# Performance work log

Measured on AMD Instinct MI355X. Metric: run time of the kernel, lower is better.

## Reference

```python
import jax, jax.numpy as jnp
import numpy as np
from math import log, ceil

BUFFER = 1
N_AHEAD = 1


def _num_weights(beta_raw):
    # matches torch: beta_max = beta.max(); min(ceil(log(0.01, beta_max)) + 1, 100)
    beta = np.asarray(jax.nn.sigmoid(beta_raw)) * 0.9999
    beta_max = float(beta.max())
    return int(min(ceil(log(0.01, beta_max)) + 1, 100))


def _garch_sigma(x, alpha_raw, beta_raw, omega_raw, num_weights, buffer, n_ahead):
    alpha = jax.nn.sigmoid(alpha_raw)          # [1, N]
    beta = jax.nn.sigmoid(beta_raw) * 0.9999   # [1, N]
    omega = jax.nn.sigmoid(omega_raw)          # [N]
    T, N = x.shape
    omega2 = omega ** 2
    w0 = omega2 / (1.0 - beta)                 # [1, N] -> GARCH long-run term
    # FIR taps: cumprod(beta)/beta then flip -> [beta^{nw-1}, ..., beta^1, beta^0]
    exps = jnp.arange(num_weights - 1, -1, -1, dtype=x.dtype)[:, None]  # [nw, 1]
    weight = beta ** exps                                               # [nw, N]
    if buffer > 0:
        weight = jnp.concatenate([weight, jnp.zeros((buffer, N), x.dtype)], axis=0)
    K = num_weights + buffer
    x2 = (x * x).T[None]                       # [1, N, T]
    kern = weight.T[:, None, :]                # [N, 1, K]  depthwise kernel
    # torch conv1d = cross-correlation; same for lax.conv_general_dilated
    a = jax.lax.conv_general_dilated(
        x2, kern, window_strides=(1,), padding=[(K - 1, K - 1)],
        dimension_numbers=('NCH', 'OIH', 'NCH'), feature_group_count=N)
    a = a[0, :, :T].T                          # [T, N] causal weighted sum of x^2
    var = w0 + alpha * a                       # [T, N]
    if n_ahead > 1:
        a_b = jax.lax.stop_gradient(jnp.clip(alpha + beta, 0.0, 0.99))
        a_b_n = a_b ** n_ahead
        co2 = (1.0 - a_b_n) / (1.0 - a_b) / n_ahead
        co1 = (1.0 - co2) / (1.0 - a_b)
        var = co1 * omega2 + co2 * var
    return jnp.sqrt(var)


def setup_inputs() -> dict:
    key = jax.random.key(0)
    k1, k2, k3, k4 = jax.random.split(key, 4)
    T, N = 8192, 2048
    x = jax.random.normal(k1, (T, N), jnp.float32) * 0.02      # daily-return scale
    alpha_raw = jax.random.uniform(k2, (1, N), jnp.float32, -4.0, -1.0)
    beta_raw = jax.random.uniform(k3, (1, N), jnp.float32, 0.0, 4.0)
    omega_raw = jax.random.uniform(k4, (N,), jnp.float32, -4.0, -2.0)
    return {"x": x, "alpha_raw": alpha_raw, "beta_raw": beta_raw, "omega_raw": omega_raw}


def reference(x, alpha_raw, beta_raw, omega_raw):
    nw = _num_weights(beta_raw)
    return _garch_sigma(x, alpha_raw, beta_raw, omega_raw, nw, BUFFER, N_AHEAD)
```

## Files before the change

kernel.cpp:

```cpp
#include <hip/hip_runtime.h>
#include <math.h>

#define TPB    256
#define COLS   32
#define SEGLEN 32
#define SEGS   8
#define HSEGS  4
#define QSEGS  (SEGS + HSEGS)
#define TSPAN  (SEGS * SEGLEN)
#define HALO   (HSEGS * SEGLEN)

__global__ __launch_bounds__(TPB, 6) void garch_sigma_kernel(
    const float* __restrict__ x,
    const float* __restrict__ alpha_raw,
    const float* __restrict__ beta_raw,
    const float* __restrict__ omega_raw,
    float*       __restrict__ out,
    int T, int N) {

    __shared__ float Qs[QSEGS][COLS];

    const int tid = threadIdx.x;
    const int col = tid & (COLS - 1);
    const int k   = tid >> 5;
    const int n   = blockIdx.x * COLS + col;
    const int t0  = blockIdx.y * TSPAN;

    const int  nc     = (n < N) ? n : (N - 1);
    const bool col_ok = (n < N);

    const float alpha = 1.f / (1.f + expf(-alpha_raw[nc]));
    const float beta  = (1.f / (1.f + expf(-beta_raw[nc]))) * 0.9999f;
    const float om    = 1.f / (1.f + expf(-omega_raw[nc]));
    const float w0    = om * om / (1.f - beta);

    const size_t rs = (size_t)N;
    const float* __restrict__ xc = x + nc;

    const int g0 = t0 + k * SEGLEN;
    float p[SEGLEN];
    if (t0 + TSPAN <= T) {
        #pragma unroll
        for (int i = 0; i < SEGLEN; ++i)
            p[i] = xc[(size_t)(g0 + i) * rs];
    } else {
        #pragma unroll
        for (int i = 0; i < SEGLEN; ++i)
            p[i] = (g0 + i < T) ? xc[(size_t)(g0 + i) * rs] : 0.f;
    }

    if (k < HSEGS) {
        const int h0 = t0 - HALO + k * SEGLEN;
        float q = 0.f;
        if (h0 >= 0) {
            #pragma unroll
            for (int b = 0; b < 2; ++b) {
                float h[16];
                #pragma unroll
                for (int i = 0; i < 16; ++i)
                    h[i] = xc[(size_t)(h0 + b * 16 + i) * rs];
                #pragma unroll
                for (int i = 0; i < 16; ++i)
                    q = fmaf(beta, q, h[i] * h[i]);
            }
        } else {
            #pragma unroll
            for (int i = 0; i < SEGLEN; ++i) {
                const int gt = h0 + i;
                const float v = (gt >= 0) ? xc[(size_t)gt * rs] : 0.f;
                q = fmaf(beta, q, v * v);
            }
        }
        Qs[k][col] = q;
    }

    {
        float q = 0.f;
        #pragma unroll
        for (int i = 0; i < SEGLEN; ++i) {
            const float s = p[i] * p[i];
            p[i] = s;
            q = fmaf(beta, q, s);
        }
        Qs[HSEGS + k][col] = q;
    }

    __syncthreads();

    float b32;
    {
        const float b2 = beta * beta;
        const float b4 = b2 * b2;
        const float b8 = b4 * b4;
        const float b16 = b8 * b8;
        b32 = b16 * b16;
    }
    float a = 0.f;
    const int nq = k + HSEGS;
    for (int u = 0; u < nq; ++u)
        a = fmaf(b32, a, Qs[u][col]);

    if (col_ok) {
        float* op = out + (size_t)g0 * rs + nc;
        if (t0 + TSPAN <= T) {
            #pragma unroll
            for (int i = 0; i < SEGLEN; ++i) {
                const float sg = sqrtf(fmaf(alpha, a, w0));
                __builtin_nontemporal_store(sg, op + (size_t)i * rs);
                a = fmaf(beta, a, p[i]);
            }
        } else {
            #pragma unroll
            for (int i = 0; i < SEGLEN; ++i) {
                const float sg = sqrtf(fmaf(alpha, a, w0));
                if (g0 + i < T)
                    __builtin_nontemporal_store(sg, op + (size_t)i * rs);
                a = fmaf(beta, a, p[i]);
            }
        }
    }
}

extern "C" void kernel_launch(void* const* d_in, const int* in_sizes, int n_in,
                              void* d_out, int out_size, void* d_ws, size_t ws_size,
                              hipStream_t stream) {
    const float* x   = (const float*)d_in[0];
    const float* ar  = (const float*)d_in[1];
    const float* br  = (const float*)d_in[2];
    const float* orw = (const float*)d_in[3];
    float* out = (float*)d_out;

    const int N = in_sizes[1];
    const int T = in_sizes[0] / N;

    dim3 grid((N + COLS - 1) / COLS, (T + TSPAN - 1) / TSPAN);
    hipLaunchKernelGGL(garch_sigma_kernel, grid, dim3(TPB), 0, stream,
                       x, ar, br, orw, out, T, N);
}
```

Measured before the change: 29.92 us.

## Double segment length and spread halo loading evenly across all warps

Each thread now processes 64 time steps instead of 32, so each block covers 512 steps and the 128-step halo is a smaller share of the loads. The halo is split into 16-step pieces, one per warp, so no warp carries extra halo work and the load stays balanced. The prefix combine uses beta^16 for halo pieces and beta^64 for body segments. In exchange, register use roughly doubles (64-element array), the occupancy hint is dropped, and the grid has half as many blocks.

```diff
diff --git a/kernel.cpp b/kernel.cpp
--- a/kernel.cpp
+++ b/kernel.cpp
@@ -1,16 +1,15 @@
 #include <hip/hip_runtime.h>
 #include <math.h>
 
-#define TPB    256
-#define COLS   32
-#define SEGLEN 32
-#define SEGS   8
-#define HSEGS  4
-#define QSEGS  (SEGS + HSEGS)
-#define TSPAN  (SEGS * SEGLEN)
-#define HALO   (HSEGS * SEGLEN)
+#define TPB     256
+#define COLS    32
+#define SEGS    8
+#define SEGLEN  64
+#define TSPAN   (SEGS * SEGLEN)
+#define HSEGLEN 16
+#define HALO    (SEGS * HSEGLEN)
 
-__global__ __launch_bounds__(TPB, 6) void garch_sigma_kernel(
+__global__ __launch_bounds__(TPB) void garch_sigma_kernel(
     const float* __restrict__ x,
     const float* __restrict__ alpha_raw,
     const float* __restrict__ beta_raw,
@@ -18,7 +17,8 @@
     float*       __restrict__ out,
     int T, int N) {
 
-    __shared__ float Qs[QSEGS][COLS];
+    __shared__ float QsH[SEGS][COLS];
+    __shared__ float QsO[SEGS][COLS];
 
     const int tid = threadIdx.x;
     const int col = tid & (COLS - 1);
@@ -37,6 +37,21 @@
     const size_t rs = (size_t)N;
     const float* __restrict__ xc = x + nc;
 
+    {
+        const int h0 = t0 - HALO + k * HSEGLEN;
+        float q = 0.f;
+        if (h0 >= 0) {
+            float h[HSEGLEN];
+            #pragma unroll
+            for (int i = 0; i < HSEGLEN; ++i)
+                h[i] = xc[(size_t)(h0 + i) * rs];
+            #pragma unroll
+            for (int i = 0; i < HSEGLEN; ++i)
+                q = fmaf(beta, q, h[i] * h[i]);
+        }
+        QsH[k][col] = q;
+    }
+
     const int g0 = t0 + k * SEGLEN;
     float p[SEGLEN];
     if (t0 + TSPAN <= T) {
@@ -48,32 +63,6 @@
         for (int i = 0; i < SEGLEN; ++i)
             p[i] = (g0 + i < T) ? xc[(size_t)(g0 + i) * rs] : 0.f;
     }
-
-    if (k < HSEGS) {
-        const int h0 = t0 - HALO + k * SEGLEN;
-        float q = 0.f;
-        if (h0 >= 0) {
-            #pragma unroll
-            for (int b = 0; b < 2; ++b) {
-                float h[16];
-                #pragma unroll
-                for (int i = 0; i < 16; ++i)
-                    h[i] = xc[(size_t)(h0 + b * 16 + i) * rs];
-                #pragma unroll
-                for (int i = 0; i < 16; ++i)
-                    q = fmaf(beta, q, h[i] * h[i]);
-            }
-        } else {
-            #pragma unroll
-            for (int i = 0; i < SEGLEN; ++i) {
-                const int gt = h0 + i;
-                const float v = (gt >= 0) ? xc[(size_t)gt * rs] : 0.f;
-                q = fmaf(beta, q, v * v);
-            }
-        }
-        Qs[k][col] = q;
-    }
-
     {
         float q = 0.f;
         #pragma unroll
@@ -82,23 +71,23 @@
             p[i] = s;
             q = fmaf(beta, q, s);
         }
-        Qs[HSEGS + k][col] = q;
+        QsO[k][col] = q;
     }
 
     __syncthreads();
 
-    float b32;
-    {
-        const float b2 = beta * beta;
-        const float b4 = b2 * b2;
-        const float b8 = b4 * b4;
-        const float b16 = b8 * b8;
-        b32 = b16 * b16;
-    }
+    const float b2  = beta * beta;
+    const float b4  = b2 * b2;
+    const float b8  = b4 * b4;
+    const float b16 = b8 * b8;
+    const float b64 = b16 * b16 * b16 * b16;
+
     float a = 0.f;
-    const int nq = k + HSEGS;
-    for (int u = 0; u < nq; ++u)
-        a = fmaf(b32, a, Qs[u][col]);
+    #pragma unroll
+    for (int u = 0; u < SEGS; ++u)
+        a = fmaf(a, b16, QsH[u][col]);
+    for (int u = 0; u < k; ++u)
+        a = fmaf(a, b64, QsO[u][col]);
 
     if (col_ok) {
         float* op = out + (size_t)g0 * rs + nc;
```

Measured after the change: 30.12 us. Within noise of the previous version (+0.7%).
